# Kernel tuning notes

Measured on AMD Instinct MI355X. Metric: run time of the kernel, lower is better.

The kernel has to match this reference:

```python
import jax, jax.numpy as jnp
import numpy as np

B, S, D, H = 4, 2048, 1024, 16
DEPTH = D // H
NEG = -1000000000.0


def setup_inputs() -> dict:
    key = jax.random.key(0)
    ks = jax.random.split(key, 11)
    scale = 1.0 / np.sqrt(D)
    return {
        "q": jax.random.normal(ks[0], (B, S, D), jnp.float32),
        "k": jax.random.normal(ks[1], (B, S, D), jnp.float32),
        "v": jax.random.normal(ks[2], (B, S, D), jnp.float32),
        "wq_w": jax.random.normal(ks[3], (D, D), jnp.float32) * scale,
        "wq_b": jax.random.normal(ks[4], (D,), jnp.float32) * 0.01,
        "wk_w": jax.random.normal(ks[5], (D, D), jnp.float32) * scale,
        "wk_b": jax.random.normal(ks[6], (D,), jnp.float32) * 0.01,
        "wv_w": jax.random.normal(ks[7], (D, D), jnp.float32) * scale,
        "wv_b": jax.random.normal(ks[8], (D,), jnp.float32) * 0.01,
        "dense_w": jax.random.normal(ks[9], (D, D), jnp.float32) * scale,
        "dense_b": jax.random.normal(ks[10], (D,), jnp.float32) * 0.01,
    }


def _split_heads(x):
    # (B, S, D) -> (B, H, S, depth)
    b, s, _ = x.shape
    return x.reshape(b, s, H, DEPTH).transpose(0, 2, 1, 3)


def reference(q, k, v, wq_w, wq_b, wk_w, wk_b, wv_w, wv_b, dense_w, dense_b):
    b, s, _ = q.shape
    qh = _split_heads(q @ wq_w.T + wq_b)
    kh = _split_heads(k @ wk_w.T + wk_b)
    vh = _split_heads(v @ wv_w.T + wv_b)
    logits = jnp.einsum('bhqd,bhkd->bhqk', qh, kh) / np.sqrt(DEPTH).astype(np.float32)
    # additive causal mask (strict upper triangle = -1e9)
    mask = jnp.where(jnp.triu(jnp.ones((s, s), jnp.float32), k=1) == 1.0, NEG, 0.0)
    logits = logits + mask
    attn = jax.nn.softmax(logits, axis=-1)
    out = jnp.einsum('bhqk,bhkd->bhqd', attn, vh)
    out = out.transpose(0, 2, 1, 3).reshape(b, s, D)
    return out @ dense_w.T + dense_b
```

## Files before the change

kernel.cpp:

```cpp
#include <hip/hip_runtime.h>
#include <hip/hip_bf16.h>


typedef __attribute__((ext_vector_type(8))) short bf16x8;
typedef __attribute__((ext_vector_type(4))) float f32x4;
typedef __attribute__((ext_vector_type(8))) unsigned short u16x8;

#define MFMA16(a, b, c) __builtin_amdgcn_mfma_f32_16x16x32_bf16(a, b, c, 0, 0, 0)

#define GLOAD_LDS16(gp, lp)                                                    \
  __builtin_amdgcn_global_load_lds(                                            \
      (const __attribute__((address_space(1))) void*)(gp),                     \
      (__attribute__((address_space(3))) void*)(lp), 16, 0, 0)

__device__ __forceinline__ unsigned short f2bf(float f) {
  union { float f; unsigned u; } x; x.f = f;
  unsigned u = x.u;
  return (unsigned short)((u + 0x7fffu + ((u >> 16) & 1u)) >> 16);
}

__device__ __forceinline__ unsigned pk2(float a, float b) {
  union { __hip_bfloat162 h; unsigned u; } cv;
  cv.h = __float22bfloat162_rn(float2{a, b});
  return cv.u;
}

__global__ __launch_bounds__(256) void convert_kernel(
    const float* __restrict__ q, const float* __restrict__ k,
    const float* __restrict__ v, const float* __restrict__ wq,
    const float* __restrict__ wk, const float* __restrict__ wv,
    const float* __restrict__ wd, const float* __restrict__ bq,
    const float* __restrict__ bk, const float* __restrict__ bv,
    unsigned short* __restrict__ dst, float* __restrict__ bias_pack) {
  const size_t tid0 = (size_t)blockIdx.x * blockDim.x + threadIdx.x;
  const size_t nthreads = (size_t)gridDim.x * blockDim.x;
  if (tid0 < 3072) {
    bias_pack[tid0] = tid0 < 1024 ? bq[tid0]
                     : (tid0 < 2048 ? bk[tid0 - 1024] : bv[tid0 - 2048]);
  }
  const size_t NQ = 8192ull * 1024;
  const size_t NW = 1024ull * 1024;
  const size_t total_chunks = (3 * NQ + 4 * NW) / 8;
  for (size_t c = tid0; c < total_chunks; c += nthreads) {
    const size_t e = c * 8;
    const float* src;
    if (e < NQ) src = q + e;
    else if (e < 2 * NQ) src = k + (e - NQ);
    else if (e < 3 * NQ) src = v + (e - 2 * NQ);
    else {
      const size_t we = e - 3 * NQ;
      if (we < NW) src = wq + we;
      else if (we < 2 * NW) src = wk + (we - NW);
      else if (we < 3 * NW) src = wv + (we - 2 * NW);
      else src = wd + (we - 3 * NW);
    }
    f32x4 a = *(const f32x4*)(src);
    f32x4 b = *(const f32x4*)(src + 4);
    u16x8 o;
    o[0] = f2bf(a[0]); o[1] = f2bf(a[1]); o[2] = f2bf(a[2]); o[3] = f2bf(a[3]);
    o[4] = f2bf(b[0]); o[5] = f2bf(b[1]); o[6] = f2bf(b[2]); o[7] = f2bf(b[3]);
    *(u16x8*)(dst + e) = o;
  }
}

template <int MODE>
__global__ __launch_bounds__(512, 2) void gemm8_kernel(
    const unsigned short* __restrict__ Abase,
    const unsigned short* __restrict__ Wbase,
    const float* __restrict__ biasbase, unsigned short* __restrict__ dstb,
    float* __restrict__ dstf) {
  __shared__ __attribute__((aligned(16))) unsigned short Ablk[3][128 * 64];
  __shared__ __attribute__((aligned(16))) unsigned short Bblk[3][256 * 64];
  const size_t NQ = 8192ull * 1024, NW = 1024ull * 1024;
  const int nx = gridDim.x, ny = gridDim.y;
  const int tot = nx * ny * (int)gridDim.z;
  int flat = ((int)blockIdx.z * ny + blockIdx.y) * nx + blockIdx.x;
  flat = (flat & 7) * (tot >> 3) + (flat >> 3);
  const int bx = flat % nx;
  const int tmp = flat / nx;
  const int by = tmp % ny;
  const int z = tmp / ny;

  const unsigned short* A;
  const unsigned short* W;
  if (MODE == 0) { A = Abase + (size_t)z * NQ; W = Wbase + (size_t)z * NW; }
  else if (MODE == 2) { A = Wbase + 2 * NW; W = Abase + 2 * NQ; }
  else { A = Abase; W = Wbase; }
  const int m0 = by * 128, n0 = bx * 256;

  const int tid = threadIdx.x, lane = tid & 63, w = tid >> 6;
  const int wm = w >> 2, wn = w & 3;
  const int llo = lane & 15, lhi = lane >> 4;

  int srcA[2], srcB[4];
#pragma unroll
  for (int j = 0; j < 4; ++j) {
    const int c = tid + j * 512;
    const int off = (c >> 3) * 1024 + ((((c & 7) ^ ((c >> 3) & 7))) << 3);
    if (j < 2) srcA[j] = off;
    srcB[j] = off;
  }
  const unsigned short* Ag = A + (size_t)m0 * 1024;
  const unsigned short* Wg = W + (size_t)n0 * 1024;

#define STA(bi, kt_, j)                                                        \
  GLOAD_LDS16(Ag + srcA[j] + (kt_) * 64,                                       \
              (unsigned short*)Ablk[bi] + (tid + (j) * 512) * 8)
#define STB(bi, kt_, j)                                                        \
  GLOAD_LDS16(Wg + srcB[j] + (kt_) * 64,                                       \
              (unsigned short*)Bblk[bi] + (tid + (j) * 512) * 8)

  f32x4 acc[4][4] = {};
  const int cswz0 = ((lhi ^ (llo & 7)) << 3);
  const int cswz1 = (((4 + lhi) ^ (llo & 7)) << 3);

  STA(0, 0, 0); STA(0, 0, 1);
  STB(0, 0, 0); STB(0, 0, 1); STB(0, 0, 2); STB(0, 0, 3);
  STA(1, 1, 0); STA(1, 1, 1);
  STB(1, 1, 0); STB(1, 1, 1); STB(1, 1, 2); STB(1, 1, 3);

#pragma unroll
  for (int kt = 0; kt < 16; ++kt) {
    const int cb = kt % 3, nb = (kt + 2) % 3;
    __builtin_amdgcn_s_barrier();
    __builtin_amdgcn_sched_barrier(0);
    if (kt + 2 < 16) { STA(nb, kt + 2, 0); STA(nb, kt + 2, 1); STB(nb, kt + 2, 0); }
    if (kt <= 13) asm volatile("s_waitcnt vmcnt(9)" ::: "memory");
    else if (kt == 14) asm volatile("s_waitcnt vmcnt(6)" ::: "memory");
    else asm volatile("s_waitcnt vmcnt(0)" ::: "memory");
    __builtin_amdgcn_s_barrier();
    __builtin_amdgcn_sched_barrier(0);

    bf16x8 af[4][2], bf01[2][2];
#pragma unroll
    for (int mi = 0; mi < 4; ++mi) {
      const int ar = (wm * 64 + mi * 16 + llo) * 64;
      af[mi][0] = *(const bf16x8*)&Ablk[cb][ar + cswz0];
      af[mi][1] = *(const bf16x8*)&Ablk[cb][ar + cswz1];
    }
#pragma unroll
    for (int ni = 0; ni < 2; ++ni) {
      const int br = (wn * 64 + ni * 16 + llo) * 64;
      bf01[ni][0] = *(const bf16x8*)&Bblk[cb][br + cswz0];
      bf01[ni][1] = *(const bf16x8*)&Bblk[cb][br + cswz1];
    }
    __builtin_amdgcn_s_setprio(1);
#pragma unroll
    for (int mi = 0; mi < 4; ++mi)
#pragma unroll
      for (int ni = 0; ni < 2; ++ni) {
        acc[mi][ni] = MFMA16(af[mi][0], bf01[ni][0], acc[mi][ni]);
        acc[mi][ni] = MFMA16(af[mi][1], bf01[ni][1], acc[mi][ni]);
      }
    __builtin_amdgcn_s_setprio(0);
    __builtin_amdgcn_s_barrier();
    __builtin_amdgcn_sched_barrier(0);

    if (kt + 2 < 16) { STB(nb, kt + 2, 1); STB(nb, kt + 2, 2); STB(nb, kt + 2, 3); }
    bf16x8 bf23[2][2];
#pragma unroll
    for (int ni = 0; ni < 2; ++ni) {
      const int br = (wn * 64 + (ni + 2) * 16 + llo) * 64;
      bf23[ni][0] = *(const bf16x8*)&Bblk[cb][br + cswz0];
      bf23[ni][1] = *(const bf16x8*)&Bblk[cb][br + cswz1];
    }
    __builtin_amdgcn_s_setprio(1);
#pragma unroll
    for (int mi = 0; mi < 4; ++mi)
#pragma unroll
      for (int ni = 0; ni < 2; ++ni) {
        acc[mi][ni + 2] = MFMA16(af[mi][0], bf23[ni][0], acc[mi][ni + 2]);
        acc[mi][ni + 2] = MFMA16(af[mi][1], bf23[ni][1], acc[mi][ni + 2]);
      }
    __builtin_amdgcn_s_setprio(0);
  }
#undef STA
#undef STB

  const float osc = (MODE == 0 && z == 0) ? 0.1803368801f : 1.0f;
  const float* bias = (MODE == 0) ? biasbase + (size_t)z * 1024
                     : (MODE == 2) ? biasbase + 2048 : biasbase;
#pragma unroll
  for (int mi = 0; mi < 4; ++mi) {
#pragma unroll
    for (int ni = 0; ni < 4; ++ni) {
      const int n = n0 + wn * 64 + ni * 16 + llo;
      const int mbase = m0 + wm * 64 + mi * 16 + lhi * 4;
#pragma unroll
      for (int r = 0; r < 4; ++r) {
        const int m = mbase + r;
        if (MODE == 1) {
          dstf[(size_t)m * 1024 + n] = acc[mi][ni][r] + bias[n];
        } else if (MODE == 0) {
          const float val = (acc[mi][ni][r] + bias[n]) * osc;
          const int b = m >> 11, s = m & 2047, h = n >> 6, d = n & 63;
          dstb[(size_t)z * NQ + (((size_t)(b * 16 + h) * 2048 + s) * 64 + d)] =
              f2bf(val);
        } else {
          const float val = acc[mi][ni][r] + bias[m];
          const int h = m >> 6, d = m & 63, b = n >> 11, sidx = n & 2047;
          const int t = sidx & 63;
          const int ps = (sidx & ~63) | ((t & 15) << 2) | (t >> 4);
          dstb[2 * NQ + (((size_t)(b * 16 + h) * 64 + d) * 2048 + ps)] =
              f2bf(val);
        }
      }
    }
  }
}

__global__ __launch_bounds__(256, 2) void attn_kernel(
    const unsigned short* __restrict__ Qp, const unsigned short* __restrict__ Kp,
    const unsigned short* __restrict__ Vtp, unsigned short* __restrict__ attn_out) {
  __shared__ __attribute__((aligned(16))) unsigned short Klds[2][64 * 64];
  __shared__ __attribute__((aligned(16))) unsigned short Vt[2][64 * 64];
  __shared__ __attribute__((aligned(16))) unsigned short Plds[4 * 32 * 72];
  const int flat = (int)blockIdx.x;
  const int xcd = flat & 7, idx = flat >> 3;
  const int bh = xcd * 8 + (idx >> 3);
  const int pr = idx & 7;
  const int tid = threadIdx.x, lane = tid & 63, w = tid >> 6;
  const int llo = lane & 15, lhi = lane >> 4;
  const int qbase[2] = {pr * 128 + w * 32, (15 - pr) * 128 + w * 32};

  bf16x8 qf[2][2][2];
#pragma unroll
  for (int t = 0; t < 2; ++t)
#pragma unroll
    for (int mi = 0; mi < 2; ++mi) {
      const unsigned short* qptr =
          Qp + ((size_t)bh * 2048 + qbase[t] + mi * 16 + llo) * 64 + lhi * 8;
      qf[t][mi][0] = *(const bf16x8*)qptr;
      qf[t][mi][1] = *(const bf16x8*)(qptr + 32);
    }

  bf16x8 ones;
#pragma unroll
  for (int i = 0; i < 8; ++i) ones[i] = (short)0x3F80;

  f32x4 o[2][2][5] = {};

  const size_t kbase = (size_t)bh * (64 * 2048);
  const int r0 = tid >> 3, r1 = r0 + 32;
  const int scb = (tid & 7) * 16;
  const int kcol0 = (scb ^ ((r0 & 7) << 4)) >> 1;
  const int kcol1 = (scb ^ ((r1 & 7) << 4)) >> 1;
  const int koff0 = r0 * 64 + kcol0, koff1 = r1 * 64 + kcol1;
  const int voff0 = r0 * 2048 + kcol0, voff1 = r1 * 2048 + kcol1;
  unsigned short* pw = &Plds[w * (32 * 72)];

  const int nkt = 2 * (16 - pr);

#define STAGE(buf, kv0_)                                                       \
  do {                                                                         \
    GLOAD_LDS16(Kp + kbase + (size_t)(kv0_)*64 + koff0, &Klds[buf][tid * 8]);  \
    GLOAD_LDS16(Kp + kbase + (size_t)(kv0_)*64 + koff1,                        \
                &Klds[buf][2048 + tid * 8]);                                   \
    GLOAD_LDS16(Vtp + kbase + (kv0_) + voff0, &Vt[buf][tid * 8]);              \
    GLOAD_LDS16(Vtp + kbase + (kv0_) + voff1, &Vt[buf][2048 + tid * 8]);       \
  } while (0)

  STAGE(0, 0);
  __syncthreads();

  for (int kt = 0; kt < nkt; ++kt) {
    const int kv0 = kt * 64;
    const int cb = kt & 1;
    if (kt + 1 < nkt) STAGE(cb ^ 1, kv0 + 64);

#pragma unroll
    for (int t = 0; t < 2; ++t) {
      const int qb = qbase[t];
      if (kv0 <= qb + 31) {
        f32x4 s[2][4] = {};
        __builtin_amdgcn_s_setprio(1);
#pragma unroll
        for (int b4 = 0; b4 < 4; ++b4) {
          const int row = b4 * 16 + llo;
          const int sw = (row & 7) << 3;
          const bf16x8 k0 =
              *(const bf16x8*)&Klds[cb][row * 64 + ((lhi * 8) ^ sw)];
          const bf16x8 k1 =
              *(const bf16x8*)&Klds[cb][row * 64 + ((32 + lhi * 8) ^ sw)];
          s[0][b4] = MFMA16(qf[t][0][0], k0, s[0][b4]);
          s[0][b4] = MFMA16(qf[t][0][1], k1, s[0][b4]);
          s[1][b4] = MFMA16(qf[t][1][0], k0, s[1][b4]);
          s[1][b4] = MFMA16(qf[t][1][1], k1, s[1][b4]);
        }
        __builtin_amdgcn_s_setprio(0);

        const bool needm = (kv0 + 63 > qb);
#pragma unroll
        for (int mi = 0; mi < 2; ++mi) {
#pragma unroll
          for (int r = 0; r < 4; ++r) {
            float sv0 = s[mi][0][r], sv1 = s[mi][1][r];
            float sv2 = s[mi][2][r], sv3 = s[mi][3][r];
            if (needm) {
              const int qrow = qb + mi * 16 + lhi * 4 + r;
              if (kv0 + llo > qrow) sv0 = -1e9f;
              if (kv0 + 16 + llo > qrow) sv1 = -1e9f;
              if (kv0 + 32 + llo > qrow) sv2 = -1e9f;
              if (kv0 + 48 + llo > qrow) sv3 = -1e9f;
            }
            const float p0 = exp2f(sv0), p1 = exp2f(sv1);
            const float p2 = exp2f(sv2), p3 = exp2f(sv3);
            const int prow = mi * 16 + lhi * 4 + r;
            *(uint2*)&pw[prow * 72 + llo * 4] =
                make_uint2(pk2(p0, p1), pk2(p2, p3));
          }
        }

        bf16x8 pa[2][2];
#pragma unroll
        for (int mi = 0; mi < 2; ++mi) {
          pa[mi][0] = *(const bf16x8*)&pw[(mi * 16 + llo) * 72 + lhi * 8];
          pa[mi][1] = *(const bf16x8*)&pw[(mi * 16 + llo) * 72 + 32 + lhi * 8];
        }
        __builtin_amdgcn_s_setprio(1);
#pragma unroll
        for (int dblk = 0; dblk < 4; ++dblk) {
          const int row = dblk * 16 + llo;
          const int sw = (row & 7) << 3;
          const bf16x8 v0 =
              *(const bf16x8*)&Vt[cb][row * 64 + ((lhi * 8) ^ sw)];
          const bf16x8 v1 =
              *(const bf16x8*)&Vt[cb][row * 64 + ((32 + lhi * 8) ^ sw)];
          o[t][0][dblk] = MFMA16(pa[0][0], v0, o[t][0][dblk]);
          o[t][0][dblk] = MFMA16(pa[0][1], v1, o[t][0][dblk]);
          o[t][1][dblk] = MFMA16(pa[1][0], v0, o[t][1][dblk]);
          o[t][1][dblk] = MFMA16(pa[1][1], v1, o[t][1][dblk]);
        }
        o[t][0][4] = MFMA16(pa[0][0], ones, o[t][0][4]);
        o[t][0][4] = MFMA16(pa[0][1], ones, o[t][0][4]);
        o[t][1][4] = MFMA16(pa[1][0], ones, o[t][1][4]);
        o[t][1][4] = MFMA16(pa[1][1], ones, o[t][1][4]);
        __builtin_amdgcn_s_setprio(0);
      }
    }

    __syncthreads();
  }
#undef STAGE

  const int b = bh >> 4, h = bh & 15;
#pragma unroll
  for (int t = 0; t < 2; ++t) {
#pragma unroll
    for (int mi = 0; mi < 2; ++mi) {
#pragma unroll
      for (int r = 0; r < 4; ++r) {
        const float inv = 1.0f / o[t][mi][4][r];
        const int qrow = qbase[t] + mi * 16 + lhi * 4 + r;
        const size_t base = ((size_t)b * 2048 + qrow) * 1024 + h * 64;
#pragma unroll
        for (int dblk = 0; dblk < 4; ++dblk)
          attn_out[base + dblk * 16 + llo] = f2bf(o[t][mi][dblk][r] * inv);
      }
    }
  }
}

extern "C" void kernel_launch(void* const* d_in, const int* in_sizes, int n_in,
                              void* d_out, int out_size, void* d_ws,
                              size_t ws_size, hipStream_t stream) {
  const float* q = (const float*)d_in[0];
  const float* k = (const float*)d_in[1];
  const float* v = (const float*)d_in[2];
  const float* wq_w = (const float*)d_in[3];
  const float* wq_b = (const float*)d_in[4];
  const float* wk_w = (const float*)d_in[5];
  const float* wk_b = (const float*)d_in[6];
  const float* wv_w = (const float*)d_in[7];
  const float* wv_b = (const float*)d_in[8];
  const float* dense_w = (const float*)d_in[9];
  const float* dense_b = (const float*)d_in[10];
  float* out = (float*)d_out;

  char* ws = (char*)d_ws;
  const size_t MB = 1024ull * 1024;
  unsigned short* qkv_bf = (unsigned short*)(ws);
  unsigned short* w_bf = (unsigned short*)(ws + 48 * MB);
  float* bias_pack = (float*)(ws + 56 * MB);
  unsigned short* qkvp = (unsigned short*)(ws + 57 * MB);
  unsigned short* attn_o = (unsigned short*)(ws + 105 * MB);
  const size_t PEL = 8192ull * 1024;

  convert_kernel<<<dim3(2048), dim3(256), 0, stream>>>(
      q, k, v, wq_w, wk_w, wv_w, dense_w, wq_b, wk_b, wv_b, qkv_bf, bias_pack);

  gemm8_kernel<0><<<dim3(4, 64, 2), dim3(512), 0, stream>>>(
      qkv_bf, w_bf, bias_pack, qkvp, nullptr);

  gemm8_kernel<2><<<dim3(32, 8, 1), dim3(512), 0, stream>>>(
      qkv_bf, w_bf, bias_pack, qkvp, nullptr);

  attn_kernel<<<dim3(512), dim3(256), 0, stream>>>(
      qkvp, qkvp + PEL, qkvp + 2 * PEL, attn_o);

  gemm8_kernel<1><<<dim3(4, 64, 1), dim3(512), 0, stream>>>(
      attn_o, w_bf + 3ull * 1024 * 1024, dense_b, nullptr, out);
}
```

Measured before the change: 200.0 us.

## Split paired causal q-tiles into one tile per block with 4-wave occupancy

The attention kernel no longer pairs a short and a long causal query tile in each block. It launches a 64x16 grid with one 128-row q-tile per block, ordered heaviest first, and raises launch bounds to 4 blocks per CU. The P staging buffer is halved and gets an XOR swizzle in place of padding, and mi is processed sequentially to cut register use. The aim is higher occupancy and better latency hiding. The risks are losing the balanced per-block work from pairing, losing the XCD-aware bh mapping (and its L2 locality), and reloading K/V tiles for more blocks.

Result: slower. 328.5 us (+64.2%).

```diff
diff --git a/kernel.cpp b/kernel.cpp
--- a/kernel.cpp
+++ b/kernel.cpp
@@ -209,36 +209,32 @@
   }
 }
 
-__global__ __launch_bounds__(256, 2) void attn_kernel(
+__global__ __launch_bounds__(256, 4) void attn_kernel(
     const unsigned short* __restrict__ Qp, const unsigned short* __restrict__ Kp,
     const unsigned short* __restrict__ Vtp, unsigned short* __restrict__ attn_out) {
   __shared__ __attribute__((aligned(16))) unsigned short Klds[2][64 * 64];
   __shared__ __attribute__((aligned(16))) unsigned short Vt[2][64 * 64];
-  __shared__ __attribute__((aligned(16))) unsigned short Plds[4 * 32 * 72];
-  const int flat = (int)blockIdx.x;
-  const int xcd = flat & 7, idx = flat >> 3;
-  const int bh = xcd * 8 + (idx >> 3);
-  const int pr = idx & 7;
+  __shared__ __attribute__((aligned(16))) unsigned short Plds[4][16 * 64];
+  const int bh = blockIdx.x;
+  const int qt = 15 - blockIdx.y;
   const int tid = threadIdx.x, lane = tid & 63, w = tid >> 6;
   const int llo = lane & 15, lhi = lane >> 4;
-  const int qbase[2] = {pr * 128 + w * 32, (15 - pr) * 128 + w * 32};
-
-  bf16x8 qf[2][2][2];
-#pragma unroll
-  for (int t = 0; t < 2; ++t)
-#pragma unroll
-    for (int mi = 0; mi < 2; ++mi) {
-      const unsigned short* qptr =
-          Qp + ((size_t)bh * 2048 + qbase[t] + mi * 16 + llo) * 64 + lhi * 8;
-      qf[t][mi][0] = *(const bf16x8*)qptr;
-      qf[t][mi][1] = *(const bf16x8*)(qptr + 32);
-    }
+  const int qbase = qt * 128 + w * 32;
+
+  bf16x8 qf[2][2];
+#pragma unroll
+  for (int mi = 0; mi < 2; ++mi) {
+    const unsigned short* qptr =
+        Qp + ((size_t)bh * 2048 + qbase + mi * 16 + llo) * 64 + lhi * 8;
+    qf[mi][0] = *(const bf16x8*)qptr;
+    qf[mi][1] = *(const bf16x8*)(qptr + 32);
+  }
 
   bf16x8 ones;
 #pragma unroll
   for (int i = 0; i < 8; ++i) ones[i] = (short)0x3F80;
 
-  f32x4 o[2][2][5] = {};
+  f32x4 o[2][5] = {};
 
   const size_t kbase = (size_t)bh * (64 * 2048);
   const int r0 = tid >> 3, r1 = r0 + 32;
@@ -247,9 +243,9 @@
   const int kcol1 = (scb ^ ((r1 & 7) << 4)) >> 1;
   const int koff0 = r0 * 64 + kcol0, koff1 = r1 * 64 + kcol1;
   const int voff0 = r0 * 2048 + kcol0, voff1 = r1 * 2048 + kcol1;
-  unsigned short* pw = &Plds[w * (32 * 72)];
-
-  const int nkt = 2 * (16 - pr);
+  unsigned short* pw = Plds[w];
+
+  const int nkt = 2 * (qt + 1);
 
 #define STAGE(buf, kv0_)                                                       \
   do {                                                                         \
@@ -268,11 +264,11 @@
     const int cb = kt & 1;
     if (kt + 1 < nkt) STAGE(cb ^ 1, kv0 + 64);
 
-#pragma unroll
-    for (int t = 0; t < 2; ++t) {
-      const int qb = qbase[t];
-      if (kv0 <= qb + 31) {
-        f32x4 s[2][4] = {};
+    if (kv0 <= qbase + 31) {
+      const bool needm = (kv0 + 63 > qbase);
+#pragma unroll
+      for (int mi = 0; mi < 2; ++mi) {
+        f32x4 s[4] = {};
         __builtin_amdgcn_s_setprio(1);
 #pragma unroll
         for (int b4 = 0; b4 < 4; ++b4) {
@@ -282,40 +278,34 @@
               *(const bf16x8*)&Klds[cb][row * 64 + ((lhi * 8) ^ sw)];
           const bf16x8 k1 =
               *(const bf16x8*)&Klds[cb][row * 64 + ((32 + lhi * 8) ^ sw)];
-          s[0][b4] = MFMA16(qf[t][0][0], k0, s[0][b4]);
-          s[0][b4] = MFMA16(qf[t][0][1], k1, s[0][b4]);
-          s[1][b4] = MFMA16(qf[t][1][0], k0, s[1][b4]);
-          s[1][b4] = MFMA16(qf[t][1][1], k1, s[1][b4]);
+          s[b4] = MFMA16(qf[mi][0], k0, s[b4]);
+          s[b4] = MFMA16(qf[mi][1], k1, s[b4]);
         }
         __builtin_amdgcn_s_setprio(0);
 
-        const bool needm = (kv0 + 63 > qb);
-#pragma unroll
-        for (int mi = 0; mi < 2; ++mi) {
-#pragma unroll
-          for (int r = 0; r < 4; ++r) {
-            float sv0 = s[mi][0][r], sv1 = s[mi][1][r];
-            float sv2 = s[mi][2][r], sv3 = s[mi][3][r];
-            if (needm) {
-              const int qrow = qb + mi * 16 + lhi * 4 + r;
-              if (kv0 + llo > qrow) sv0 = -1e9f;
-              if (kv0 + 16 + llo > qrow) sv1 = -1e9f;
-              if (kv0 + 32 + llo > qrow) sv2 = -1e9f;
-              if (kv0 + 48 + llo > qrow) sv3 = -1e9f;
-            }
-            const float p0 = exp2f(sv0), p1 = exp2f(sv1);
-            const float p2 = exp2f(sv2), p3 = exp2f(sv3);
-            const int prow = mi * 16 + lhi * 4 + r;
-            *(uint2*)&pw[prow * 72 + llo * 4] =
-                make_uint2(pk2(p0, p1), pk2(p2, p3));
+#pragma unroll
+        for (int r = 0; r < 4; ++r) {
+          float sv0 = s[0][r], sv1 = s[1][r];
+          float sv2 = s[2][r], sv3 = s[3][r];
+          if (needm) {
+            const int qrow = qbase + mi * 16 + lhi * 4 + r;
+            if (kv0 + llo > qrow) sv0 = -1e9f;
+            if (kv0 + 16 + llo > qrow) sv1 = -1e9f;
+            if (kv0 + 32 + llo > qrow) sv2 = -1e9f;
+            if (kv0 + 48 + llo > qrow) sv3 = -1e9f;
           }
-        }
-
-        bf16x8 pa[2][2];
-#pragma unroll
-        for (int mi = 0; mi < 2; ++mi) {
-          pa[mi][0] = *(const bf16x8*)&pw[(mi * 16 + llo) * 72 + lhi * 8];
-          pa[mi][1] = *(const bf16x8*)&pw[(mi * 16 + llo) * 72 + 32 + lhi * 8];
+          const float p0 = exp2f(sv0), p1 = exp2f(sv1);
+          const float p2 = exp2f(sv2), p3 = exp2f(sv3);
+          const int prow = lhi * 4 + r;
+          const int g = llo ^ ((prow & 7) << 1);
+          *(uint2*)&pw[prow * 64 + g * 4] = make_uint2(pk2(p0, p1), pk2(p2, p3));
+        }
+
+        bf16x8 pa[2];
+#pragma unroll
+        for (int h = 0; h < 2; ++h) {
+          const int gp = ((h * 8 + lhi * 2) ^ ((llo & 7) << 1));
+          pa[h] = *(const bf16x8*)&pw[llo * 64 + gp * 4];
         }
         __builtin_amdgcn_s_setprio(1);
 #pragma unroll
@@ -326,15 +316,11 @@
               *(const bf16x8*)&Vt[cb][row * 64 + ((lhi * 8) ^ sw)];
           const bf16x8 v1 =
               *(const bf16x8*)&Vt[cb][row * 64 + ((32 + lhi * 8) ^ sw)];
-          o[t][0][dblk] = MFMA16(pa[0][0], v0, o[t][0][dblk]);
-          o[t][0][dblk] = MFMA16(pa[0][1], v1, o[t][0][dblk]);
-          o[t][1][dblk] = MFMA16(pa[1][0], v0, o[t][1][dblk]);
-          o[t][1][dblk] = MFMA16(pa[1][1], v1, o[t][1][dblk]);
-        }
-        o[t][0][4] = MFMA16(pa[0][0], ones, o[t][0][4]);
-        o[t][0][4] = MFMA16(pa[0][1], ones, o[t][0][4]);
-        o[t][1][4] = MFMA16(pa[1][0], ones, o[t][1][4]);
-        o[t][1][4] = MFMA16(pa[1][1], ones, o[t][1][4]);
+          o[mi][dblk] = MFMA16(pa[0], v0, o[mi][dblk]);
+          o[mi][dblk] = MFMA16(pa[1], v1, o[mi][dblk]);
+        }
+        o[mi][4] = MFMA16(pa[0], ones, o[mi][4]);
+        o[mi][4] = MFMA16(pa[1], ones, o[mi][4]);
         __builtin_amdgcn_s_setprio(0);
       }
     }
@@ -345,18 +331,15 @@
 
   const int b = bh >> 4, h = bh & 15;
 #pragma unroll
-  for (int t = 0; t < 2; ++t) {
-#pragma unroll
-    for (int mi = 0; mi < 2; ++mi) {
-#pragma unroll
-      for (int r = 0; r < 4; ++r) {
-        const float inv = 1.0f / o[t][mi][4][r];
-        const int qrow = qbase[t] + mi * 16 + lhi * 4 + r;
-        const size_t base = ((size_t)b * 2048 + qrow) * 1024 + h * 64;
-#pragma unroll
-        for (int dblk = 0; dblk < 4; ++dblk)
-          attn_out[base + dblk * 16 + llo] = f2bf(o[t][mi][dblk][r] * inv);
-      }
+  for (int mi = 0; mi < 2; ++mi) {
+#pragma unroll
+    for (int r = 0; r < 4; ++r) {
+      const float inv = 1.0f / o[mi][4][r];
+      const int qrow = qbase + mi * 16 + lhi * 4 + r;
+      const size_t base = ((size_t)b * 2048 + qrow) * 1024 + h * 64;
+#pragma unroll
+      for (int dblk = 0; dblk < 4; ++dblk)
+        attn_out[base + dblk * 16 + llo] = f2bf(o[mi][dblk][r] * inv);
     }
   }
 }
@@ -395,7 +378,7 @@
   gemm8_kernel<2><<<dim3(32, 8, 1), dim3(512), 0, stream>>>(
       qkv_bf, w_bf, bias_pack, qkvp, nullptr);
 
-  attn_kernel<<<dim3(512), dim3(256), 0, stream>>>(
+  attn_kernel<<<dim3(64, 16), dim3(256), 0, stream>>>(
       qkvp, qkvp + PEL, qkvp + 2 * PEL, attn_o);
 
   gemm8_kernel<1><<<dim3(4, 64, 1), dim3(512), 0, stream>>>(
```
